# Kernel optimization log

Hardware: AMD Instinct MI355X
Metric: run time of the kernel (lower is better)

## Reference

```python
import jax, jax.numpy as jnp
import numpy as np
import math

N_HEADS = 12  # from init_kwargs


def setup_inputs() -> dict:
    key = jax.random.key(0)
    ks = jax.random.split(key, 9)
    B, N, D = 32, 577, 768
    s = 1.0 / math.sqrt(D)
    return {
        "x": jax.random.normal(ks[0], (B, N, D), jnp.float32),
        "Wq": jax.random.normal(ks[1], (D, D), jnp.float32) * s,
        "bq": jax.random.normal(ks[2], (D,), jnp.float32) * 0.02,
        "Wk": jax.random.normal(ks[3], (D, D), jnp.float32) * s,
        "bk": jax.random.normal(ks[4], (D,), jnp.float32) * 0.02,
        "Wv": jax.random.normal(ks[5], (D, D), jnp.float32) * s,
        "bv": jax.random.normal(ks[6], (D,), jnp.float32) * 0.02,
        "Wo": jax.random.normal(ks[7], (D, D), jnp.float32) * s,
        "bo": jax.random.normal(ks[8], (D,), jnp.float32) * 0.02,
    }


def reference(x, Wq, bq, Wk, bk, Wv, bv, Wo, bo):
    B, N, D = x.shape
    H = N_HEADS
    Hd = D // H
    # project then split heads (intended semantics of the torch module)
    q = (x @ Wq.T + bq).reshape(B, N, H, Hd)
    k = (x @ Wk.T + bk).reshape(B, N, H, Hd)
    v = (x @ Wv.T + bv).reshape(B, N, H, Hd)
    # NOTE: faithful quirk - scale by sqrt(d_size), not sqrt(head_dim)
    scores = jnp.einsum('bqhd,bkhd->bhqk', q, k) / math.sqrt(D)  # [B,H,N,N]
    # faithful quirk: mask = triu(ones); positions where mask==0 (strictly
    # lower triangle, k < q) are filled with float32 min -> anti-causal mask
    allowed = jnp.triu(jnp.ones((N, N), dtype=bool))
    scores = jnp.where(allowed, scores, jnp.finfo(jnp.float32).min)
    att = jax.nn.softmax(scores, axis=3)  # dropout p=0.0 -> identity
    out = jnp.einsum('bhqk,bkhd->bqhd', att, v).reshape(B, N, D)
    return out @ Wo.T + bo
```

## Files before the change

kernel.cpp:

```cpp
#include <hip/hip_runtime.h>
#include <cstdint>
#include <cstddef>


typedef __bf16 bf16;
typedef __bf16 bf16x4 __attribute__((ext_vector_type(4)));
typedef __bf16 bf16x8 __attribute__((ext_vector_type(8)));
typedef float  f32x4  __attribute__((ext_vector_type(4)));

#define DEVI __device__ __forceinline__

constexpr int BATCH = 32;
constexpr int NSEQ  = 577;
constexpr int DMODEL= 768;
constexpr int NHEAD = 12;
constexpr int HD    = 64;
constexpr int M_ROWS = BATCH * NSEQ;
constexpr int M_PAD  = 145 * 128;
constexpr int N_PAD  = 640;
constexpr int QKV_N  = 3 * DMODEL;
constexpr float QSCALE = 0.036084391824351615f * 1.4426950408889634f;

DEVI void async_copy16(const void* g, void* l) {
  void* gg = (void*)(uintptr_t)g;
  __builtin_amdgcn_global_load_lds(
      (__attribute__((address_space(1))) void*)gg,
      (__attribute__((address_space(3))) void*)l,
      16, 0, 0);
}

DEVI f32x4 mfma16(bf16x8 a, bf16x8 b, f32x4 c) {
  return __builtin_amdgcn_mfma_f32_16x16x32_bf16(a, b, c, 0, 0, 0);
}

__global__ __launch_bounds__(256) void cast_kernel(
    const float* __restrict__ x,
    const float* __restrict__ wq, const float* __restrict__ wk,
    const float* __restrict__ wv, const float* __restrict__ wo,
    bf16* __restrict__ xb, bf16* __restrict__ wcat, bf16* __restrict__ wob)
{
  constexpr int XQ = (M_ROWS * DMODEL) / 4;
  constexpr int WQ = (DMODEL * DMODEL) / 4;
  int idx = blockIdx.x * 256 + threadIdx.x;
  const float4* src; bf16* dst; int off;
  if (idx < XQ) { src = (const float4*)x; dst = xb; off = idx; }
  else {
    int u = idx - XQ; int w = u / WQ; off = u - w * WQ;
    src = (const float4*)(w == 0 ? wq : w == 1 ? wk : w == 2 ? wv : wo);
    dst = (w < 3) ? (wcat + (size_t)w * DMODEL * DMODEL) : wob;
  }
  float4 v = src[off];
  bf16x4 o;
  o[0] = (bf16)v.x; o[1] = (bf16)v.y; o[2] = (bf16)v.z; o[3] = (bf16)v.w;
  *(bf16x4*)(dst + (size_t)off * 4) = o;
}

template <int MODE>
__global__ __launch_bounds__(256) void gemm_bt(
    const bf16* __restrict__ A, const bf16* __restrict__ Bw,
    const float* __restrict__ bias0, const float* __restrict__ bias1,
    const float* __restrict__ bias2,
    float* __restrict__ Cout,
    bf16* __restrict__ Qb, bf16* __restrict__ Kb, bf16* __restrict__ Vb)
{
  __shared__ __align__(16) char smem[65536];
  const int t = threadIdx.x;
  const int w = t >> 6, lane = t & 63;
  const int g = lane >> 4, cl = lane & 15;
  const int wm = (w >> 1) * 64, wn = (w & 1) * 64;

  constexpr int GX  = (MODE == 0 ? QKV_N : DMODEL) / 128;
  constexpr int NWG = GX * (M_PAD / 128);
  constexpr int QC  = NWG / 8, RC = NWG % 8;
  const int l   = blockIdx.y * GX + blockIdx.x;
  const int xcd = l & 7, pos = l >> 3;
  const int nl  = (xcd < RC ? xcd * (QC + 1) : RC * (QC + 1) + (xcd - RC) * QC) + pos;
  const int m0  = (nl / GX) * 128, n0 = (nl % GX) * 128;

  f32x4 acc[4][4] = {};

  const int srow = t >> 3;
  const int scol = ((t & 7) ^ (srow & 7)) * 8;
  const bf16* Ag = A  + (size_t)(m0 + srow) * 768 + scol;
  const bf16* Bg = Bw + (size_t)(n0 + srow) * 768 + scol;

  constexpr int NSTEP = 768 / 64;
  auto stage = [&](int st, int buf) {
    char* lA = smem + buf * 32768 + w * 1024;
    char* lB = smem + buf * 32768 + 16384 + w * 1024;
#pragma unroll
    for (int c = 0; c < 4; ++c) {
      async_copy16(Ag + st * 64 + (size_t)c * 32 * 768, lA + c * 4096);
      async_copy16(Bg + st * 64 + (size_t)c * 32 * 768, lB + c * 4096);
    }
  };

  stage(0, 0);
  __syncthreads();

  for (int st = 0; st < NSTEP; ++st) {
    const int cur = st & 1;
    if (st + 1 < NSTEP) stage(st + 1, cur ^ 1);
    const bf16* As = (const bf16*)(smem + cur * 32768);
    const bf16* Bs = (const bf16*)(smem + cur * 32768 + 16384);
#pragma unroll
    for (int ks = 0; ks < 2; ++ks) {
      const int ch = ((ks * 4 + g) ^ (cl & 7)) * 8;
      bf16x8 af[4], bfr[4];
#pragma unroll
      for (int i = 0; i < 4; ++i)
        af[i] = *(const bf16x8*)(As + (wm + i * 16 + cl) * 64 + ch);
#pragma unroll
      for (int j = 0; j < 4; ++j)
        bfr[j] = *(const bf16x8*)(Bs + (wn + j * 16 + cl) * 64 + ch);
#pragma unroll
      for (int i = 0; i < 4; ++i)
#pragma unroll
        for (int j = 0; j < 4; ++j)
          acc[i][j] = mfma16(af[i], bfr[j], acc[i][j]);
    }
    __syncthreads();
  }

  if constexpr (MODE == 0) {
    bf16* Cs = (bf16*)smem;
#pragma unroll
    for (int p = 0; p < 2; ++p) {
      __syncthreads();
      if ((w & 1) == p) {
#pragma unroll
        for (int j = 0; j < 4; ++j) {
          const int n = n0 + wn + j * 16 + cl;
          const int which = n >= 1536 ? 2 : (n >= 768 ? 1 : 0);
          const int rem = n - which * 768;
          const float bias =
              (which == 0 ? bias0 : which == 1 ? bias1 : bias2)[rem];
          const float sc = which == 0 ? QSCALE : 1.0f;
#pragma unroll
          for (int i = 0; i < 4; ++i)
#pragma unroll
            for (int r = 0; r < 4; ++r)
              Cs[(wm + i * 16 + g * 4 + r) * 72 + j * 16 + cl] =
                  (bf16)((acc[i][j][r] + bias) * sc);
        }
      }
      __syncthreads();
      const int nbase = n0 + p * 64;
      const int which = nbase >= 1536 ? 2 : (nbase >= 768 ? 1 : 0);
      const int rem0 = nbase - which * 768;
      const int h = rem0 >> 6;
      bf16* dst = which == 0 ? Qb : which == 1 ? Kb : Vb;
      const int row = t >> 1, colh = (t & 1) * 32;
      const unsigned m = (unsigned)(m0 + row);
      if (m < (unsigned)M_ROWS) {
        const unsigned bb = m / 577u;
        const unsigned nq = m - bb * 577u;
        bf16* dr = dst + ((size_t)(bb * NHEAD + h) * N_PAD + nq) * HD + colh;
        const bf16* sr = Cs + row * 72 + colh;
#pragma unroll
        for (int cc = 0; cc < 4; ++cc)
          *(bf16x8*)(dr + cc * 8) = *(const bf16x8*)(sr + cc * 8);
      }
    }
  } else {
#pragma unroll
    for (int j = 0; j < 4; ++j) {
      const int n = n0 + wn + j * 16 + cl;
      const float bias = bias0[n];
#pragma unroll
      for (int i = 0; i < 4; ++i) {
#pragma unroll
        for (int r = 0; r < 4; ++r) {
          const unsigned m = (unsigned)(m0 + wm + i * 16 + g * 4 + r);
          if (m < (unsigned)M_ROWS)
            Cout[(size_t)m * 768 + n] = acc[i][j][r] + bias;
        }
      }
    }
  }
}

__global__ __launch_bounds__(256) void transpose_v(
    const bf16* __restrict__ Vb, bf16* __restrict__ Vt)
{
  __shared__ __align__(16) bf16 Ls[64 * 72];
  const int t = threadIdx.x;
  const int bh = blockIdx.y, n0 = blockIdx.x * 64;

  const int nrow = n0 + (t >> 3);
  const bf16* src = Vb + ((size_t)bh * N_PAD + nrow) * HD + (t & 7) * 8;
  const bf16x8 z = {};
  bf16x8 a0 = (nrow      < NSEQ) ? *(const bf16x8*)src                      : z;
  bf16x8 a1 = (nrow + 32 < NSEQ) ? *(const bf16x8*)(src + (size_t)32 * HD)  : z;
  *(bf16x8*)(Ls + (t >> 3) * 72 + (t & 7) * 8) = a0;
  *(bf16x8*)(Ls + ((t >> 3) + 32) * 72 + (t & 7) * 8) = a1;
  __syncthreads();

  const int d = t >> 2, nc = (t & 3) * 16;
  bf16 o[16];
#pragma unroll
  for (int e = 0; e < 16; ++e) o[e] = Ls[(nc + e) * 72 + d];
  bf16* dst = Vt + ((size_t)bh * HD + d) * N_PAD + n0 + nc;
  *(bf16x8*)dst = *(bf16x8*)o;
  *(bf16x8*)(dst + 8) = *(bf16x8*)(o + 8);
}

__global__ __launch_bounds__(256) void attn_kernel(
    const bf16* __restrict__ Qb, const bf16* __restrict__ Kb,
    const bf16* __restrict__ Vtb, bf16* __restrict__ Ao)
{
  __shared__ __align__(16) bf16 Ks[2][64 * 64];
  __shared__ __align__(16) bf16 Vs[2][64 * 64];
  __shared__ __align__(16) bf16 Ps[4 * 32 * 64];

  const int t = threadIdx.x, w = t >> 6, lane = t & 63;
  const int g = lane >> 4, cl = lane & 15;
  const int qt = blockIdx.x;
  const int bh = blockIdx.y;
  const size_t kqbase = (size_t)bh * (N_PAD * HD);
  const size_t vbase  = (size_t)bh * (HD * N_PAD);

  const int srow = t >> 3;
  const int scol = ((t & 7) ^ (srow & 7)) * 8;

  const bf16* Kg = Kb  + kqbase + (size_t)srow * HD + scol;
  const bf16* Vg = Vtb + vbase  + (size_t)srow * N_PAD + scol;

  const int jb0 = 2 * qt, nit = 10 - jb0;

  bf16x8 aq[2][2];
#pragma unroll
  for (int ks = 0; ks < 2; ++ks)
#pragma unroll
    for (int f = 0; f < 2; ++f)
      aq[f][ks] = *(const bf16x8*)(
          Qb + kqbase + (size_t)(qt * 128 + w * 32 + f * 16 + cl) * HD +
          (ks * 4 + g) * 8);

#pragma unroll
  for (int c = 0; c < 2; ++c) {
    async_copy16(Kg + (size_t)(jb0 * 64 + c * 32) * HD,  (char*)Ks[0] + c * 4096 + w * 1024);
    async_copy16(Vg + jb0 * 64 + (size_t)(c * 32) * N_PAD, (char*)Vs[0] + c * 4096 + w * 1024);
  }
  __syncthreads();

  f32x4 oacc[2][4] = {};
  f32x4 lsum[2] = {};
  bf16x8 onesf;
#pragma unroll
  for (int e = 0; e < 8; ++e) onesf[e] = (bf16)(cl == 0 ? 1.0f : 0.0f);

  bf16* pw = Ps + w * 2048;
  const int qw0 = qt * 128 + w * 32;

  for (int it = 0; it < nit; ++it) {
    const int jb = jb0 + it;
    const int buf = it & 1;
    if (it + 1 < nit) {
      const int jn = jb + 1, nb = buf ^ 1;
#pragma unroll
      for (int c = 0; c < 2; ++c) {
        async_copy16(Kg + (size_t)(jn * 64 + c * 32) * HD,   (char*)Ks[nb] + c * 4096 + w * 1024);
        async_copy16(Vg + jn * 64 + (size_t)(c * 32) * N_PAD, (char*)Vs[nb] + c * 4096 + w * 1024);
      }
    }

    f32x4 s[2][4] = {};
    __builtin_amdgcn_s_setprio(1);
#pragma unroll
    for (int ks = 0; ks < 2; ++ks) {
      const int chk = ((ks * 4 + g) ^ (cl & 7)) * 8;
#pragma unroll
      for (int j = 0; j < 4; ++j) {
        bf16x8 bk = *(const bf16x8*)(Ks[buf] + (j * 16 + cl) * 64 + chk);
#pragma unroll
        for (int f = 0; f < 2; ++f)
          s[f][j] = mfma16(bk, aq[f][ks], s[f][j]);
      }
    }
    __builtin_amdgcn_s_setprio(0);

    float p[2][4][4];
    const bool need_mask = (jb * 64 < qw0 + 32) || (jb == 9);
    if (need_mask) {
#pragma unroll
      for (int f = 0; f < 2; ++f) {
        const int qglob = qw0 + f * 16 + cl;
#pragma unroll
        for (int j = 0; j < 4; ++j) {
#pragma unroll
          for (int r = 0; r < 4; ++r) {
            const int kg = jb * 64 + j * 16 + g * 4 + r;
            const bool ok = (kg >= qglob) && (kg < NSEQ);
            p[f][j][r] = ok ? exp2f(s[f][j][r]) : 0.f;
          }
        }
      }
    } else {
#pragma unroll
      for (int f = 0; f < 2; ++f)
#pragma unroll
        for (int j = 0; j < 4; ++j)
#pragma unroll
          for (int r = 0; r < 4; ++r)
            p[f][j][r] = exp2f(s[f][j][r]);
    }

#pragma unroll
    for (int f = 0; f < 2; ++f) {
      const int prow = f * 16 + cl;
      bf16* pr = pw + prow * 64;
      const int rk = prow & 7;
#pragma unroll
      for (int j = 0; j < 4; ++j) {
        const int c = j * 2 + (g >> 1);
        bf16x4 tmp;
#pragma unroll
        for (int r = 0; r < 4; ++r) tmp[r] = (bf16)p[f][j][r];
        *(bf16x4*)(pr + ((c ^ rk) * 8) + (g & 1) * 4) = tmp;
      }
    }

#pragma unroll
    for (int ks = 0; ks < 2; ++ks) {
      const int chp = ((ks * 4 + g) ^ (cl & 7)) * 8;
      bf16x8 ap[2], bv[4];
#pragma unroll
      for (int f = 0; f < 2; ++f)
        ap[f] = *(const bf16x8*)(pw + (f * 16 + cl) * 64 + chp);
#pragma unroll
      for (int j = 0; j < 4; ++j)
        bv[j] = *(const bf16x8*)(Vs[buf] + (j * 16 + cl) * 64 + chp);
      __builtin_amdgcn_s_setprio(1);
#pragma unroll
      for (int f = 0; f < 2; ++f) {
#pragma unroll
        for (int j = 0; j < 4; ++j)
          oacc[f][j] = mfma16(ap[f], bv[j], oacc[f][j]);
        lsum[f] = mfma16(ap[f], onesf, lsum[f]);
      }
      __builtin_amdgcn_s_setprio(0);
    }
    __syncthreads();
  }

  const int b_ = bh / NHEAD, h_ = bh - (bh / NHEAD) * NHEAD;
#pragma unroll
  for (int f = 0; f < 2; ++f)
#pragma unroll
    for (int r = 0; r < 4; ++r) {
      const int qg = qw0 + f * 16 + g * 4 + r;
      const float l = __shfl(lsum[f][r], lane & 48, 64);
      if (qg >= NSEQ) continue;
      const float inv = 1.f / l;
      const size_t row = ((size_t)b_ * NSEQ + qg) * DMODEL + h_ * HD;
#pragma unroll
      for (int j = 0; j < 4; ++j)
        Ao[row + j * 16 + cl] = (bf16)(oacc[f][j][r] * inv);
    }
}

extern "C" void kernel_launch(void* const* d_in, const int* in_sizes, int n_in,
                              void* d_out, int out_size, void* d_ws, size_t ws_size,
                              hipStream_t stream) {
  const float* x  = (const float*)d_in[0];
  const float* Wq = (const float*)d_in[1];
  const float* bq = (const float*)d_in[2];
  const float* Wk = (const float*)d_in[3];
  const float* bk = (const float*)d_in[4];
  const float* Wv = (const float*)d_in[5];
  const float* bv = (const float*)d_in[6];
  const float* Wo = (const float*)d_in[7];
  const float* bo = (const float*)d_in[8];

  char* ws = (char*)d_ws;
  size_t off = 0;
  auto alloc = [&](size_t bytes) -> char* {
    char* p = ws + off;
    off += (bytes + 255) & ~(size_t)255;
    return p;
  };
  bf16* xb   = (bf16*)alloc((size_t)M_PAD * DMODEL * 2);
  bf16* wcat = (bf16*)alloc((size_t)QKV_N * DMODEL * 2);
  bf16* wob  = (bf16*)alloc((size_t)DMODEL * DMODEL * 2);
  bf16* Qb   = (bf16*)alloc((size_t)BATCH * NHEAD * N_PAD * HD * 2);
  bf16* Kb   = (bf16*)alloc((size_t)BATCH * NHEAD * N_PAD * HD * 2);
  bf16* Vb   = (bf16*)alloc((size_t)BATCH * NHEAD * N_PAD * HD * 2);
  bf16* Vtb  = (bf16*)alloc((size_t)BATCH * NHEAD * HD * N_PAD * 2);
  bf16* Ao   = (bf16*)alloc((size_t)M_PAD * DMODEL * 2);
  (void)ws_size; (void)in_sizes; (void)n_in; (void)out_size;

  constexpr int XQ = (M_ROWS * DMODEL) / 4;
  constexpr int WQ = (DMODEL * DMODEL) / 4;
  const int cast_blocks = (XQ + 4 * WQ) / 256;
  cast_kernel<<<cast_blocks, 256, 0, stream>>>(x, Wq, Wk, Wv, Wo, xb, wcat, wob);

  gemm_bt<0><<<dim3(QKV_N / 128, M_PAD / 128), 256, 0, stream>>>(
      xb, wcat, bq, bk, bv, nullptr, Qb, Kb, Vb);

  transpose_v<<<dim3(N_PAD / 64, BATCH * NHEAD), 256, 0, stream>>>(Vb, Vtb);

  attn_kernel<<<dim3(5, BATCH * NHEAD), 256, 0, stream>>>(Qb, Kb, Vtb, Ao);

  gemm_bt<1><<<dim3(DMODEL / 128, M_PAD / 128), 256, 0, stream>>>(
      Ao, wob, bo, nullptr, nullptr, (float*)d_out, nullptr, nullptr, nullptr);
}
```

Baseline: 340.5 us.

## Deepen GEMM pipeline to 4-stage ring with 32-wide K slices and vmcnt waits

Measured after the change: 354.8 us. 1.04x slower.

```diff
diff --git a/kernel.cpp b/kernel.cpp
--- a/kernel.cpp
+++ b/kernel.cpp
@@ -79,47 +79,46 @@
 
   f32x4 acc[4][4] = {};
 
-  const int srow = t >> 3;
-  const int scol = ((t & 7) ^ (srow & 7)) * 8;
+  const int srow = t >> 2;
+  const int scol = ((t & 3) ^ (srow & 3)) * 8;
   const bf16* Ag = A  + (size_t)(m0 + srow) * 768 + scol;
   const bf16* Bg = Bw + (size_t)(n0 + srow) * 768 + scol;
 
-  constexpr int NSTEP = 768 / 64;
-  auto stage = [&](int st, int buf) {
-    char* lA = smem + buf * 32768 + w * 1024;
-    char* lB = smem + buf * 32768 + 16384 + w * 1024;
-#pragma unroll
-    for (int c = 0; c < 4; ++c) {
-      async_copy16(Ag + st * 64 + (size_t)c * 32 * 768, lA + c * 4096);
-      async_copy16(Bg + st * 64 + (size_t)c * 32 * 768, lB + c * 4096);
-    }
+  constexpr int SUBS = 768 / 32;
+  auto stage = [&](int sub) {
+    char* base = smem + (sub & 3) * 16384 + w * 1024;
+    const size_t ko = (size_t)sub * 32;
+    async_copy16(Ag + ko,                    base);
+    async_copy16(Ag + ko + (size_t)64 * 768, base + 4096);
+    async_copy16(Bg + ko,                    base + 8192);
+    async_copy16(Bg + ko + (size_t)64 * 768, base + 12288);
   };
 
-  stage(0, 0);
-  __syncthreads();
-
-  for (int st = 0; st < NSTEP; ++st) {
-    const int cur = st & 1;
-    if (st + 1 < NSTEP) stage(st + 1, cur ^ 1);
-    const bf16* As = (const bf16*)(smem + cur * 32768);
-    const bf16* Bs = (const bf16*)(smem + cur * 32768 + 16384);
-#pragma unroll
-    for (int ks = 0; ks < 2; ++ks) {
-      const int ch = ((ks * 4 + g) ^ (cl & 7)) * 8;
-      bf16x8 af[4], bfr[4];
-#pragma unroll
-      for (int i = 0; i < 4; ++i)
-        af[i] = *(const bf16x8*)(As + (wm + i * 16 + cl) * 64 + ch);
+  stage(0); stage(1); stage(2);
+
+#pragma unroll
+  for (int s = 0; s < SUBS; ++s) {
+    if (s <= SUBS - 3)      asm volatile("s_waitcnt vmcnt(8)" ::: "memory");
+    else if (s == SUBS - 2) asm volatile("s_waitcnt vmcnt(4)" ::: "memory");
+    else                    asm volatile("s_waitcnt vmcnt(0)" ::: "memory");
+    __builtin_amdgcn_s_barrier();
+    if (s + 3 < SUBS) stage(s + 3);
+
+    const bf16* As = (const bf16*)(smem + (s & 3) * 16384);
+    const bf16* Bs = (const bf16*)(smem + (s & 3) * 16384 + 8192);
+    const int ch = (g ^ (cl & 3)) * 8;
+    bf16x8 af[4], bfr[4];
+#pragma unroll
+    for (int i = 0; i < 4; ++i)
+      af[i] = *(const bf16x8*)(As + (wm + i * 16 + cl) * 32 + ch);
+#pragma unroll
+    for (int j = 0; j < 4; ++j)
+      bfr[j] = *(const bf16x8*)(Bs + (wn + j * 16 + cl) * 32 + ch);
+#pragma unroll
+    for (int i = 0; i < 4; ++i)
 #pragma unroll
       for (int j = 0; j < 4; ++j)
-        bfr[j] = *(const bf16x8*)(Bs + (wn + j * 16 + cl) * 64 + ch);
-#pragma unroll
-      for (int i = 0; i < 4; ++i)
-#pragma unroll
-        for (int j = 0; j < 4; ++j)
-          acc[i][j] = mfma16(af[i], bfr[j], acc[i][j]);
-    }
-    __syncthreads();
+        acc[i][j] = mfma16(af[i], bfr[j], acc[i][j]);
   }
 
   if constexpr (MODE == 0) {
```
